# Kernel optimization log

Measured on AMD Instinct MI355X. Metric: run time of the kernel, lower is better.

## Reference

```python
import jax, jax.numpy as jnp
import numpy as np
import math

V, E, H, NL = 10000, 256, 512, 2
B, T = 64, 128


def _lstm_cell(x, h, c, Wih, Whh, b):
    # PyTorch gate order: i, f, g, o
    gates = x @ Wih.T + h @ Whh.T + b
    i, f, g, o = jnp.split(gates, 4, axis=-1)
    c = jax.nn.sigmoid(f) * c + jax.nn.sigmoid(i) * jnp.tanh(g)
    h = jax.nn.sigmoid(o) * jnp.tanh(c)
    return h, c


def _run_layer(xs, Wih, Whh, b):
    # xs: [T, B, D]; returns outputs [T, B, H] and final (h, c)
    Bn = xs.shape[1]
    h0 = jnp.zeros((Bn, H), xs.dtype)
    c0 = jnp.zeros((Bn, H), xs.dtype)

    def step(carry, x):
        h, c = carry
        h, c = _lstm_cell(x, h, c, Wih, Whh, b)
        return (h, c), h

    (hT, cT), ys = jax.lax.scan(step, (h0, c0), xs)
    return ys, hT, cT


def setup_inputs() -> dict:
    key = jax.random.key(0)
    ks = jax.random.split(key, 24)
    s = 0.05

    def n(k, shape):
        return jax.random.normal(k, shape, dtype=jnp.float32) * s

    inp = {
        "input_ids": jax.random.randint(ks[0], (B, T), 0, V),
        "my_attention_mask": jax.random.randint(ks[1], (B, T), 0, 2),
        "update_step": 1000,
        # encoder params
        "enc_embed": n(ks[2], (V, E)),
        "enc_Wih0": n(ks[3], (4 * H, E)),
        "enc_Whh0": n(ks[4], (4 * H, H)),
        "enc_b0": n(ks[5], (4 * H,)),
        "enc_Wih1": n(ks[6], (4 * H, H)),
        "enc_Whh1": n(ks[7], (4 * H, H)),
        "enc_b1": n(ks[8], (4 * H,)),
        # decoder params
        "dec_embed": n(ks[9], (V, E)),
        "dec_Wih0": n(ks[10], (4 * H, E)),
        "dec_Whh0": n(ks[11], (4 * H, H)),
        "dec_b0": n(ks[12], (4 * H,)),
        "dec_Wih1": n(ks[13], (4 * H, H)),
        "dec_Whh1": n(ks[14], (4 * H, H)),
        "dec_b1": n(ks[15], (4 * H,)),
        "dec_Wout": n(ks[16], (V, H)),
        "dec_bout": n(ks[17], (V,)),
    }
    return inp


def _forward(input_ids, my_attention_mask, update_step,
             enc_embed, enc_Wih0, enc_Whh0, enc_b0, enc_Wih1, enc_Whh1, enc_b1,
             dec_embed, dec_Wih0, dec_Whh0, dec_b0, dec_Wih1, dec_Whh1, dec_b1,
             dec_Wout, dec_bout):
    temp_ids = input_ids.T                      # [T, B]
    mask = my_attention_mask                    # [B, T]

    # ---- encoder: 2-layer LSTM over the full sequence ----
    emb = enc_embed[temp_ids]                   # [T, B, E]
    ys0, h0, c0 = _run_layer(emb, enc_Wih0, enc_Whh0, enc_b0)
    _, h1, c1 = _run_layer(ys0, enc_Wih1, enc_Whh1, enc_b1)

    def dec_step(carry, tok):
        dh0, dc0, dh1, dc1 = carry
        x = dec_embed[tok]                      # [B, E]
        dh0, dc0 = _lstm_cell(x, dh0, dc0, dec_Wih0, dec_Whh0, dec_b0)
        dh1, dc1 = _lstm_cell(dh0, dh1, dc1, dec_Wih1, dec_Whh1, dec_b1)
        out = dh1 @ dec_Wout.T + dec_bout       # [B, V]
        return (dh0, dc0, dh1, dc1), out

    _, dec_outs = jax.lax.scan(dec_step, (h0, c0, h1, c1), temp_ids[:-1])  # [T-1, B, V]

    # ---- mask-driven compaction: outputs[i, j] = dec_out at t where
    #      i = exclusive-cumsum of mask[j, :t]; unwritten slots stay random ----
    outputs = jax.random.uniform(jax.random.key(42), (T, B, V), dtype=jnp.float32)
    idx = jnp.cumsum(mask, axis=1) - mask       # exclusive cumsum, [B, T]
    write_i = jnp.where(mask[:, 1:] > 0, idx[:, 1:], T)   # OOB -> dropped
    vals = jnp.transpose(dec_outs, (1, 0, 2))   # [B, T-1, V]
    outputs = outputs.at[write_i, jnp.arange(B)[:, None]].set(vals, mode="drop")

    # ---- hard gumbel-softmax with straight-through ----
    temperature = max(0.5, math.exp(-0.003 * update_step))
    eps = 1e-20
    U = jax.random.uniform(jax.random.key(7), (T, B, V), dtype=jnp.float32)
    g = -jnp.log(-jnp.log(U + eps) + eps)
    y = jax.nn.softmax((outputs + g) / temperature, axis=-1)
    y_hard = jax.nn.one_hot(jnp.argmax(y, axis=-1), V, dtype=y.dtype)
    gs = jax.lax.stop_gradient(y_hard - y) + y  # [T, B, V]

    # ---- scatter back into padded layout: masked positions pull compacted
    #      gumbel onehots, unmasked positions get onehot(input id) ----
    gathered = gs[jnp.clip(idx, 0, T - 1), jnp.arange(B)[:, None]]  # [B, T, V]
    id_onehot = jax.nn.one_hot(input_ids, V, dtype=jnp.float32)     # [B, T, V]
    onehots = jnp.where((mask > 0)[:, :, None], gathered, id_onehot)
    return onehots.reshape(B * T, V)


def reference(input_ids, my_attention_mask, update_step,
              enc_embed, enc_Wih0, enc_Whh0, enc_b0, enc_Wih1, enc_Whh1, enc_b1,
              dec_embed, dec_Wih0, dec_Whh0, dec_b0, dec_Wih1, dec_Whh1, dec_b1,
              dec_Wout, dec_bout):
    return _forward(input_ids, my_attention_mask, update_step,
                    enc_embed, enc_Wih0, enc_Whh0, enc_b0, enc_Wih1, enc_Whh1, enc_b1,
                    dec_embed, dec_Wih0, dec_Whh0, dec_b0, dec_Wih1, dec_Whh1, dec_b1,
                    dec_Wout, dec_bout)
```

## Files before the change

kernel.cpp:

```cpp
#include <hip/hip_runtime.h>
#include <stdint.h>


#define RNG_VARIANT 2

__device__ __forceinline__ void threefry2x32(uint32_t k0, uint32_t k1,
                                             uint32_t x0, uint32_t x1,
                                             uint32_t& o0, uint32_t& o1)
{
  const uint32_t k2 = k0 ^ k1 ^ 0x1BD11BDAu;
  x0 += k0; x1 += k1;
#define TF_R(r) x0 += x1; x1 = (x1 << r) | (x1 >> (32 - r)); x1 ^= x0;
  TF_R(13) TF_R(15) TF_R(26) TF_R(6)
  x0 += k1; x1 += k2 + 1u;
  TF_R(17) TF_R(29) TF_R(16) TF_R(24)
  x0 += k2; x1 += k0 + 2u;
  TF_R(13) TF_R(15) TF_R(26) TF_R(6)
  x0 += k0; x1 += k1 + 3u;
  TF_R(17) TF_R(29) TF_R(16) TF_R(24)
  x0 += k1; x1 += k2 + 4u;
  TF_R(13) TF_R(15) TF_R(26) TF_R(6)
  x0 += k2; x1 += k0 + 5u;
#undef TF_R
  o0 = x0; o1 = x1;
}

__device__ __forceinline__ float jax_uniform(uint32_t seed, uint32_t i)
{
  uint32_t bits;
#if RNG_VARIANT == 0
  const uint32_t HALF = 40960000u;
  const bool lo = (i < HALF);
  const uint32_t x0 = lo ? i : (i - HALF);
  uint32_t o0, o1;
  threefry2x32(0u, seed, x0, x0 + HALF, o0, o1);
  bits = lo ? o0 : o1;
#else
  uint32_t o0, o1;
  threefry2x32(0u, seed, 0u, i, o0, o1);
#if RNG_VARIANT == 1
  bits = o1;
#elif RNG_VARIANT == 2
  bits = o0 ^ o1;
#else
  bits = o0;
#endif
#endif
  return __uint_as_float(0x3F800000u | (bits >> 9)) - 1.0f;
}

__global__ __launch_bounds__(256)
void gemm_kernel(const float* __restrict__ A, const int* __restrict__ ids,
                 const float* __restrict__ W, const float* __restrict__ bias,
                 float* __restrict__ C, int M, int N, int K, int amode, int cmode)
{
  __shared__ __align__(16) float As[16][64];
  __shared__ __align__(16) float Bs[16][64];
  const int tid = threadIdx.x;
  const int tx = tid & 15;
  const int ty = tid >> 4;
  const int m0 = blockIdx.x * 64;
  const int n0 = blockIdx.y * 64;
  const int lm = tid >> 2;
  const int kq = tid & 3;

  const float* arow = nullptr;
  if (amode == 0) {
    const int m = m0 + lm;
    const int token = ids[(m & 63) * 128 + (m >> 6)];
    arow = A + (size_t)token * K;
  }
  const int nW = n0 + lm;
  const bool wok = (nW < N);
  const float* wrow = W + (size_t)(wok ? nW : 0) * K;

  float acc[4][4] = {{0.f,0.f,0.f,0.f},{0.f,0.f,0.f,0.f},
                     {0.f,0.f,0.f,0.f},{0.f,0.f,0.f,0.f}};

  for (int k0 = 0; k0 < K; k0 += 16) {
    if (amode == 0) {
      const float4 av = *(const float4*)(arow + k0 + kq * 4);
      As[kq*4+0][lm] = av.x; As[kq*4+1][lm] = av.y;
      As[kq*4+2][lm] = av.z; As[kq*4+3][lm] = av.w;
    } else {
      ((float4*)&As[0][0])[tid] =
          ((const float4*)(A + (size_t)m0 * K + (size_t)k0 * 64))[tid];
    }
    float4 wv = make_float4(0.f, 0.f, 0.f, 0.f);
    if (wok) wv = *(const float4*)(wrow + k0 + kq * 4);
    Bs[kq*4+0][lm] = wv.x; Bs[kq*4+1][lm] = wv.y;
    Bs[kq*4+2][lm] = wv.z; Bs[kq*4+3][lm] = wv.w;
    __syncthreads();
#pragma unroll
    for (int kk = 0; kk < 16; ++kk) {
      const float4 a4 = *(const float4*)&As[kk][ty * 4];
      const float4 b4 = *(const float4*)&Bs[kk][tx * 4];
      acc[0][0] += a4.x*b4.x; acc[0][1] += a4.x*b4.y; acc[0][2] += a4.x*b4.z; acc[0][3] += a4.x*b4.w;
      acc[1][0] += a4.y*b4.x; acc[1][1] += a4.y*b4.y; acc[1][2] += a4.y*b4.z; acc[1][3] += a4.y*b4.w;
      acc[2][0] += a4.z*b4.x; acc[2][1] += a4.z*b4.y; acc[2][2] += a4.z*b4.z; acc[2][3] += a4.z*b4.w;
      acc[3][0] += a4.w*b4.x; acc[3][1] += a4.w*b4.y; acc[3][2] += a4.w*b4.z; acc[3][3] += a4.w*b4.w;
    }
    __syncthreads();
  }

  if (cmode == 0) {
#pragma unroll
    for (int i = 0; i < 4; ++i) {
      const int m = m0 + ty * 4 + i;
#pragma unroll
      for (int j = 0; j < 4; ++j) {
        const int n = n0 + tx * 4 + j;
        if (n < N) C[(size_t)m * N + n] = acc[i][j] + bias[n];
      }
    }
  } else {
    float* cb = C + (size_t)m0 * N;
#pragma unroll
    for (int j = 0; j < 4; ++j) {
      const int n = n0 + tx * 4 + j;
      if (n < N) {
        const float bv = bias[n];
#pragma unroll
        for (int i = 0; i < 4; ++i)
          cb[(size_t)n * 64 + ty * 4 + i] = acc[i][j] + bv;
      }
    }
  }
}

__global__ __launch_bounds__(128)
void lstm_step_kernel(const float* __restrict__ Xg,
                      const float* __restrict__ hprev,
                      const float* __restrict__ Whh,
                      float* __restrict__ cstate,
                      float* __restrict__ hout)
{
  __shared__ __align__(16) float ws[8][512];
  __shared__ __align__(16) float hs[4096];
  const int tid = threadIdx.x;
  const int b = tid & 63;
  const int ui = tid >> 6;
  const int U0 = blockIdx.x * 2;
  const int u = U0 + ui;

  {
    const int r = tid >> 4;
    const int lui = r >> 2, lg = r & 3;
    const float* wrow = Whh + (size_t)(lg * 512 + U0 + lui) * 512;
    const int kq = tid & 15;
#pragma unroll
    for (int i = 0; i < 8; ++i) {
      const int k = kq * 4 + i * 64;
      *(float4*)&ws[r][k] = *(const float4*)(wrow + k);
    }
  }

  const float x_i = Xg[(size_t)(0 * 512 + u) * 64 + b];
  const float x_f = Xg[(size_t)(1 * 512 + u) * 64 + b];
  const float x_g = Xg[(size_t)(2 * 512 + u) * 64 + b];
  const float x_o = Xg[(size_t)(3 * 512 + u) * 64 + b];
  const float c_old = cstate[(size_t)u * 64 + b];

  float4 pre[8];
#pragma unroll
  for (int i = 0; i < 8; ++i) pre[i] = ((const float4*)hprev)[tid + 128 * i];

  float a0 = 0.f, a1 = 0.f, a2 = 0.f, a3 = 0.f;
  for (int kc = 0; kc < 8; ++kc) {
    __syncthreads();
#pragma unroll
    for (int i = 0; i < 8; ++i) ((float4*)hs)[tid + 128 * i] = pre[i];
    __syncthreads();
    if (kc < 7) {
#pragma unroll
      for (int i = 0; i < 8; ++i)
        pre[i] = ((const float4*)hprev)[(kc + 1) * 1024 + tid + 128 * i];
    }
    const int kb = kc * 64;
#pragma unroll
    for (int kg = 0; kg < 16; ++kg) {
      const float h0 = hs[(kg * 4 + 0) * 64 + b];
      const float h1 = hs[(kg * 4 + 1) * 64 + b];
      const float h2 = hs[(kg * 4 + 2) * 64 + b];
      const float h3 = hs[(kg * 4 + 3) * 64 + b];
      const float4 w0 = *(const float4*)&ws[ui * 4 + 0][kb + kg * 4];
      const float4 w1 = *(const float4*)&ws[ui * 4 + 1][kb + kg * 4];
      const float4 w2 = *(const float4*)&ws[ui * 4 + 2][kb + kg * 4];
      const float4 w3 = *(const float4*)&ws[ui * 4 + 3][kb + kg * 4];
      a0 += h0 * w0.x + h1 * w0.y + h2 * w0.z + h3 * w0.w;
      a1 += h0 * w1.x + h1 * w1.y + h2 * w1.z + h3 * w1.w;
      a2 += h0 * w2.x + h1 * w2.y + h2 * w2.z + h3 * w2.w;
      a3 += h0 * w3.x + h1 * w3.y + h2 * w3.z + h3 * w3.w;
    }
  }

  const float zi = x_i + a0, zf = x_f + a1, zg = x_g + a2, zo = x_o + a3;
  const float I = 1.0f / (1.0f + expf(-zi));
  const float F = 1.0f / (1.0f + expf(-zf));
  const float G = tanhf(zg);
  const float O = 1.0f / (1.0f + expf(-zo));
  const float cn = F * c_old + I * G;
  cstate[(size_t)u * 64 + b] = cn;
  hout[(size_t)u * 64 + b] = O * tanhf(cn);
}

__global__ __launch_bounds__(256)
void token_kernel(const int* __restrict__ input_ids,
                  const int* __restrict__ mask,
                  const float* __restrict__ logits,
                  int* __restrict__ tokens)
{
  const int row = blockIdx.x;
  const int b = row >> 7;
  const int t = row & 127;
  const int tid = threadIdx.x;
  const int mk = mask[row];
  if (mk == 0) {
    if (tid == 0) tokens[row] = input_ids[row];
    return;
  }
  int r = 0;
  for (int s = 0; s < t; ++s) r += mask[(b << 7) + s];

  const uint32_t base7  = (uint32_t)(r * 64 + b) * 10000u;
  const uint32_t base42 = (uint32_t)b * 10000u;
  const size_t loff = (t >= 1) ? (size_t)((t - 1) * 64 + b) * 10000u : 0u;
  const float* lrow = logits + loff;

  float best = -3.0e38f;
  int bestv = 0;
  for (int v = tid; v < 10000; v += 256) {
    const float u7 = jax_uniform(7u, base7 + (uint32_t)v);
    const float g = -logf(-logf(u7 + 1e-20f) + 1e-20f);
    float z = (t >= 1) ? lrow[v] : jax_uniform(42u, base42 + (uint32_t)v);
    z += g;
    if (z > best) { best = z; bestv = v; }
  }
  __shared__ float sv[256];
  __shared__ int sidx[256];
  sv[tid] = best; sidx[tid] = bestv;
  __syncthreads();
  for (int s = 128; s > 0; s >>= 1) {
    if (tid < s) {
      const float ov = sv[tid + s]; const int oi = sidx[tid + s];
      if (ov > sv[tid] || (ov == sv[tid] && oi < sidx[tid])) {
        sv[tid] = ov; sidx[tid] = oi;
      }
    }
    __syncthreads();
  }
  if (tid == 0) tokens[row] = sidx[0];
}

__global__ __launch_bounds__(256)
void onehot_kernel(const int* __restrict__ tokens, float* __restrict__ out)
{
  const int row = blockIdx.x;
  const int tok = tokens[row];
  float4* orow = (float4*)(out + (size_t)row * 10000);
  for (int q = threadIdx.x; q < 2500; q += 256) {
    float4 v = make_float4(0.f, 0.f, 0.f, 0.f);
    const int v0 = q << 2;
    const unsigned d = (unsigned)(tok - v0);
    if (d < 4u) ((float*)&v)[d] = 1.0f;
    orow[q] = v;
  }
}

__global__ __launch_bounds__(256)
void zero_kernel(float* __restrict__ p, int n)
{
  const int i = blockIdx.x * 256 + threadIdx.x;
  if (i < n) p[i] = 0.f;
}

extern "C" void kernel_launch(void* const* d_in, const int* in_sizes, int n_in,
                              void* d_out, int out_size, void* d_ws, size_t ws_size,
                              hipStream_t stream)
{
  const int*   input_ids = (const int*)d_in[0];
  const int*   mask      = (const int*)d_in[1];
  const float* enc_embed = (const float*)d_in[3];
  const float* enc_Wih0  = (const float*)d_in[4];
  const float* enc_Whh0  = (const float*)d_in[5];
  const float* enc_b0    = (const float*)d_in[6];
  const float* enc_Wih1  = (const float*)d_in[7];
  const float* enc_Whh1  = (const float*)d_in[8];
  const float* enc_b1    = (const float*)d_in[9];
  const float* dec_embed = (const float*)d_in[10];
  const float* dec_Wih0  = (const float*)d_in[11];
  const float* dec_Whh0  = (const float*)d_in[12];
  const float* dec_b0    = (const float*)d_in[13];
  const float* dec_Wih1  = (const float*)d_in[14];
  const float* dec_Whh1  = (const float*)d_in[15];
  const float* dec_b1    = (const float*)d_in[16];
  const float* dec_Wout  = (const float*)d_in[17];
  const float* dec_bout  = (const float*)d_in[18];

  float* outf = (float*)d_out;
  float* Xg   = outf;
  float* seqA = (float*)d_ws;
  float* zbuf = seqA + (size_t)128 * 32768;
  float* cA   = zbuf + 32768;
  float* cB   = cA + 32768;
  float* hp0  = cB + 32768;
  float* hp1  = hp0 + 32768;
  int* tokens = (int*)(hp1 + 32768);

  zero_kernel<<<384, 256, 0, stream>>>(zbuf, 3 * 32768);

  gemm_kernel<<<dim3(128, 32), 256, 0, stream>>>(
      enc_embed, input_ids, enc_Wih0, enc_b0, Xg, 8192, 2048, 256, 0, 1);
  for (int t = 0; t < 128; ++t) {
    const float* hi = (t == 0) ? zbuf : (seqA + (size_t)(t - 1) * 32768);
    lstm_step_kernel<<<256, 128, 0, stream>>>(
        Xg + (size_t)t * 131072, hi, enc_Whh0, cA, seqA + (size_t)t * 32768);
  }

  gemm_kernel<<<dim3(128, 32), 256, 0, stream>>>(
      seqA, nullptr, enc_Wih1, enc_b1, Xg, 8192, 2048, 512, 1, 1);
  for (int t = 0; t < 128; ++t) {
    const float* hi = (t == 0) ? zbuf : ((t & 1) ? hp0 : hp1);
    float* ho = (t & 1) ? hp1 : hp0;
    lstm_step_kernel<<<256, 128, 0, stream>>>(
        Xg + (size_t)t * 131072, hi, enc_Whh1, cB, ho);
  }

  gemm_kernel<<<dim3(127, 32), 256, 0, stream>>>(
      dec_embed, input_ids, dec_Wih0, dec_b0, Xg, 8128, 2048, 256, 0, 1);
  for (int j = 0; j < 127; ++j) {
    const float* hi = (j == 0) ? (seqA + (size_t)127 * 32768)
                               : (seqA + (size_t)(j - 1) * 32768);
    lstm_step_kernel<<<256, 128, 0, stream>>>(
        Xg + (size_t)j * 131072, hi, dec_Whh0, cA, seqA + (size_t)j * 32768);
  }

  gemm_kernel<<<dim3(127, 32), 256, 0, stream>>>(
      seqA, nullptr, dec_Wih1, dec_b1, Xg, 8128, 2048, 512, 1, 1);
  for (int j = 0; j < 127; ++j) {
    const float* hi = (j == 0) ? hp1 : (seqA + (size_t)(j - 1) * 32768);
    lstm_step_kernel<<<256, 128, 0, stream>>>(
        Xg + (size_t)j * 131072, hi, dec_Whh1, cB, seqA + (size_t)j * 32768);
  }

  gemm_kernel<<<dim3(127, 157), 256, 0, stream>>>(
      seqA, nullptr, dec_Wout, dec_bout, outf, 8128, 10000, 512, 1, 0);

  token_kernel<<<8192, 256, 0, stream>>>(input_ids, mask, outf, tokens);
  onehot_kernel<<<8192, 256, 0, stream>>>(tokens, outf);
}
```

Baseline: 12.85 ms.

## Use split-bf16 MFMA GEMMs and fuse Gumbel argmax into output projection

Replaces the fp32 SIMT GEMMs with MFMA bf16 GEMMs that split each fp32 operand into hi/lo bf16 parts and use three products to keep near-fp32 accuracy. The hidden-state sequences are transposed and split, and the weights and embeddings are pre-split every call. The output projection GEMM now fuses the Gumbel noise and argmax, combining per-tile winners through packed 64-bit atomicMax keys. This removes the 8128x10000 logits write and re-read and the separate token kernel. In exchange it adds split and transpose passes on every call, and tie-breaking or precision may differ slightly.

```diff
diff --git a/kernel.cpp b/kernel.cpp
--- a/kernel.cpp
+++ b/kernel.cpp
@@ -2,7 +2,8 @@
 #include <stdint.h>
 
 
-#define RNG_VARIANT 2
+typedef short bf16x8 __attribute__((ext_vector_type(8)));
+typedef float f32x4 __attribute__((ext_vector_type(4)));
 
 __device__ __forceinline__ void threefry2x32(uint32_t k0, uint32_t k1,
                                              uint32_t x0, uint32_t x1,
@@ -27,102 +28,187 @@
 
 __device__ __forceinline__ float jax_uniform(uint32_t seed, uint32_t i)
 {
-  uint32_t bits;
-#if RNG_VARIANT == 0
-  const uint32_t HALF = 40960000u;
-  const bool lo = (i < HALF);
-  const uint32_t x0 = lo ? i : (i - HALF);
-  uint32_t o0, o1;
-  threefry2x32(0u, seed, x0, x0 + HALF, o0, o1);
-  bits = lo ? o0 : o1;
-#else
   uint32_t o0, o1;
   threefry2x32(0u, seed, 0u, i, o0, o1);
-#if RNG_VARIANT == 1
-  bits = o1;
-#elif RNG_VARIANT == 2
-  bits = o0 ^ o1;
-#else
-  bits = o0;
-#endif
-#endif
+  const uint32_t bits = o0 ^ o1;
   return __uint_as_float(0x3F800000u | (bits >> 9)) - 1.0f;
 }
 
-__global__ __launch_bounds__(256)
-void gemm_kernel(const float* __restrict__ A, const int* __restrict__ ids,
-                 const float* __restrict__ W, const float* __restrict__ bias,
-                 float* __restrict__ C, int M, int N, int K, int amode, int cmode)
-{
-  __shared__ __align__(16) float As[16][64];
-  __shared__ __align__(16) float Bs[16][64];
+__device__ __forceinline__ ushort f2bf(float x)
+{
+  const uint32_t u = __float_as_uint(x);
+  const uint32_t r = u + 0x7FFFu + ((u >> 16) & 1u);
+  return (ushort)(r >> 16);
+}
+__device__ __forceinline__ float bf2f(ushort b)
+{
+  return __uint_as_float(((uint32_t)b) << 16);
+}
+
+__device__ __forceinline__ unsigned long long packkey(float f, int n)
+{
+  uint32_t u = __float_as_uint(f);
+  u = (u & 0x80000000u) ? ~u : (u | 0x80000000u);
+  return ((unsigned long long)u << 32) | (uint32_t)(0x7FFFFFFF - n);
+}
+
+__global__ __launch_bounds__(256)
+void split_kernel(const float* __restrict__ src, ushort* __restrict__ hi,
+                  ushort* __restrict__ lo, int n)
+{
+  const int i = blockIdx.x * 256 + threadIdx.x;
+  if (i < n) {
+    const float v = src[i];
+    const ushort h = f2bf(v);
+    hi[i] = h;
+    lo[i] = f2bf(v - bf2f(h));
+  }
+}
+
+__global__ __launch_bounds__(256)
+void transpose_split_kernel(const float* __restrict__ seq,
+                            ushort* __restrict__ Thi, ushort* __restrict__ Tlo)
+{
+  __shared__ float tile[128][65];
+  const int t = blockIdx.x >> 2;
+  const int kc = blockIdx.x & 3;
   const int tid = threadIdx.x;
-  const int tx = tid & 15;
-  const int ty = tid >> 4;
-  const int m0 = blockIdx.x * 64;
-  const int n0 = blockIdx.y * 64;
-  const int lm = tid >> 2;
-  const int kq = tid & 3;
-
-  const float* arow = nullptr;
-  if (amode == 0) {
-    const int m = m0 + lm;
-    const int token = ids[(m & 63) * 128 + (m >> 6)];
-    arow = A + (size_t)token * K;
-  }
-  const int nW = n0 + lm;
-  const bool wok = (nW < N);
-  const float* wrow = W + (size_t)(wok ? nW : 0) * K;
-
-  float acc[4][4] = {{0.f,0.f,0.f,0.f},{0.f,0.f,0.f,0.f},
-                     {0.f,0.f,0.f,0.f},{0.f,0.f,0.f,0.f}};
-
-  for (int k0 = 0; k0 < K; k0 += 16) {
-    if (amode == 0) {
-      const float4 av = *(const float4*)(arow + k0 + kq * 4);
-      As[kq*4+0][lm] = av.x; As[kq*4+1][lm] = av.y;
-      As[kq*4+2][lm] = av.z; As[kq*4+3][lm] = av.w;
+  const float* sbase = seq + (size_t)t * 32768 + (size_t)kc * 128 * 64;
+#pragma unroll
+  for (int it = 0; it < 32; ++it) {
+    const int idx = it * 256 + tid;
+    tile[idx >> 6][idx & 63] = sbase[idx];
+  }
+  __syncthreads();
+#pragma unroll
+  for (int it = 0; it < 32; ++it) {
+    const int idx = it * 256 + tid;
+    const int b = idx >> 7, k = idx & 127;
+    const float v = tile[k][b];
+    const size_t o = ((size_t)t * 64 + b) * 512 + kc * 128 + k;
+    const ushort h = f2bf(v);
+    Thi[o] = h;
+    Tlo[o] = f2bf(v - bf2f(h));
+  }
+}
+
+template <int GATHER, int FUSED>
+__global__ __launch_bounds__(256)
+void gemm_split(const ushort* __restrict__ Ahi, const ushort* __restrict__ Alo,
+                const int* __restrict__ ids,
+                const ushort* __restrict__ Whi, const ushort* __restrict__ Wlo,
+                const float* __restrict__ bias, float* __restrict__ Xg,
+                const int* __restrict__ mask, const int* __restrict__ idxmap,
+                unsigned long long* __restrict__ keys,
+                int M, int N, int K)
+{
+  const int tid = threadIdx.x;
+  const int wid = tid >> 6, lane = tid & 63;
+  const int lm = lane & 15, quad = lane >> 4;
+  const int m0 = blockIdx.x * 128 + (wid >> 1) * 64;
+  const int n0 = blockIdx.y * 128 + (wid & 1) * 64;
+  const int koff = quad * 8;
+
+  size_t offA[4];
+#pragma unroll
+  for (int mi = 0; mi < 4; ++mi) {
+    int m = m0 + mi * 16 + lm;
+    int mc = m < M ? m : (M - 1);
+    if (GATHER) {
+      const int tok = ids[(mc & 63) * 128 + (mc >> 6)];
+      offA[mi] = (size_t)tok * K;
     } else {
-      ((float4*)&As[0][0])[tid] =
-          ((const float4*)(A + (size_t)m0 * K + (size_t)k0 * 64))[tid];
-    }
-    float4 wv = make_float4(0.f, 0.f, 0.f, 0.f);
-    if (wok) wv = *(const float4*)(wrow + k0 + kq * 4);
-    Bs[kq*4+0][lm] = wv.x; Bs[kq*4+1][lm] = wv.y;
-    Bs[kq*4+2][lm] = wv.z; Bs[kq*4+3][lm] = wv.w;
-    __syncthreads();
-#pragma unroll
-    for (int kk = 0; kk < 16; ++kk) {
-      const float4 a4 = *(const float4*)&As[kk][ty * 4];
-      const float4 b4 = *(const float4*)&Bs[kk][tx * 4];
-      acc[0][0] += a4.x*b4.x; acc[0][1] += a4.x*b4.y; acc[0][2] += a4.x*b4.z; acc[0][3] += a4.x*b4.w;
-      acc[1][0] += a4.y*b4.x; acc[1][1] += a4.y*b4.y; acc[1][2] += a4.y*b4.z; acc[1][3] += a4.y*b4.w;
-      acc[2][0] += a4.z*b4.x; acc[2][1] += a4.z*b4.y; acc[2][2] += a4.z*b4.z; acc[2][3] += a4.z*b4.w;
-      acc[3][0] += a4.w*b4.x; acc[3][1] += a4.w*b4.y; acc[3][2] += a4.w*b4.z; acc[3][3] += a4.w*b4.w;
-    }
-    __syncthreads();
-  }
-
-  if (cmode == 0) {
-#pragma unroll
-    for (int i = 0; i < 4; ++i) {
-      const int m = m0 + ty * 4 + i;
-#pragma unroll
-      for (int j = 0; j < 4; ++j) {
-        const int n = n0 + tx * 4 + j;
-        if (n < N) C[(size_t)m * N + n] = acc[i][j] + bias[n];
+      offA[mi] = (size_t)mc * K;
+    }
+  }
+  size_t offB[4];
+#pragma unroll
+  for (int ni = 0; ni < 4; ++ni) {
+    int n = n0 + ni * 16 + lm;
+    int nc = n < N ? n : (N - 1);
+    offB[ni] = (size_t)nc * K;
+  }
+
+  f32x4 acc[4][4];
+#pragma unroll
+  for (int mi = 0; mi < 4; ++mi)
+#pragma unroll
+    for (int ni = 0; ni < 4; ++ni) acc[mi][ni] = (f32x4){0.f, 0.f, 0.f, 0.f};
+
+  for (int k0 = 0; k0 < K; k0 += 32) {
+    bf16x8 ah[4], al[4];
+#pragma unroll
+    for (int mi = 0; mi < 4; ++mi) {
+      ah[mi] = *(const bf16x8*)(Ahi + offA[mi] + k0 + koff);
+      al[mi] = *(const bf16x8*)(Alo + offA[mi] + k0 + koff);
+    }
+#pragma unroll
+    for (int ni = 0; ni < 4; ++ni) {
+      const bf16x8 bh = *(const bf16x8*)(Whi + offB[ni] + k0 + koff);
+      const bf16x8 bl = *(const bf16x8*)(Wlo + offB[ni] + k0 + koff);
+#pragma unroll
+      for (int mi = 0; mi < 4; ++mi) {
+        acc[mi][ni] = __builtin_amdgcn_mfma_f32_16x16x32_bf16(ah[mi], bl, acc[mi][ni], 0, 0, 0);
+        acc[mi][ni] = __builtin_amdgcn_mfma_f32_16x16x32_bf16(al[mi], bh, acc[mi][ni], 0, 0, 0);
+        acc[mi][ni] = __builtin_amdgcn_mfma_f32_16x16x32_bf16(ah[mi], bh, acc[mi][ni], 0, 0, 0);
       }
     }
+  }
+
+  float bv[4];
+#pragma unroll
+  for (int ni = 0; ni < 4; ++ni) {
+    int n = n0 + ni * 16 + lm;
+    bv[ni] = bias[n < N ? n : (N - 1)];
+  }
+
+  if (FUSED == 0) {
+#pragma unroll
+    for (int mi = 0; mi < 4; ++mi) {
+#pragma unroll
+      for (int i = 0; i < 4; ++i) {
+        const int m = m0 + mi * 16 + quad * 4 + i;
+        if (m >= M) continue;
+        const int t = m >> 6, b = m & 63;
+        float* base = Xg + (size_t)t * 131072 + b;
+#pragma unroll
+        for (int ni = 0; ni < 4; ++ni) {
+          const int n = n0 + ni * 16 + lm;
+          base[(size_t)n * 64] = acc[mi][ni][i] + bv[ni];
+        }
+      }
+    }
   } else {
-    float* cb = C + (size_t)m0 * N;
-#pragma unroll
-    for (int j = 0; j < 4; ++j) {
-      const int n = n0 + tx * 4 + j;
-      if (n < N) {
-        const float bv = bias[n];
-#pragma unroll
-        for (int i = 0; i < 4; ++i)
-          cb[(size_t)n * 64 + ty * 4 + i] = acc[i][j] + bv;
+#pragma unroll
+    for (int mi = 0; mi < 4; ++mi) {
+#pragma unroll
+      for (int i = 0; i < 4; ++i) {
+        const int m = m0 + mi * 16 + quad * 4 + i;
+        if (m >= M) continue;
+        const int j = m >> 6, b = m & 63;
+        const int outrow = b * 128 + j + 1;
+        if (mask[outrow] == 0) continue;
+        const int r = idxmap[outrow];
+        const uint32_t base7 = (uint32_t)(r * 64 + b) * 10000u;
+        float best = -3.0e38f;
+        int bestn = 0;
+#pragma unroll
+        for (int ni = 0; ni < 4; ++ni) {
+          const int n = n0 + ni * 16 + lm;
+          if (n < N) {
+            const float u7 = jax_uniform(7u, base7 + (uint32_t)n);
+            const float g = -logf(-logf(u7 + 1e-20f) + 1e-20f);
+            const float z = acc[mi][ni][i] + bv[ni] + g;
+            if (z > best) { best = z; bestn = n; }
+          }
+        }
+        unsigned long long key = packkey(best, bestn);
+#pragma unroll
+        for (int s = 1; s < 16; s <<= 1) {
+          const unsigned long long o = __shfl_xor(key, s, 64);
+          if (o > key) key = o;
+        }
+        if (lm == 0) atomicMax(keys + outrow, key);
       }
     }
   }
@@ -204,52 +290,55 @@
   hout[(size_t)u * 64 + b] = O * tanhf(cn);
 }
 
-__global__ __launch_bounds__(256)
-void token_kernel(const int* __restrict__ input_ids,
-                  const int* __restrict__ mask,
-                  const float* __restrict__ logits,
-                  int* __restrict__ tokens)
-{
-  const int row = blockIdx.x;
-  const int b = row >> 7;
-  const int t = row & 127;
+__global__ void maskscan_kernel(const int* __restrict__ mask,
+                                int* __restrict__ idxmap)
+{
+  const int b = threadIdx.x;
+  int run = 0;
+  for (int t = 0; t < 128; ++t) {
+    idxmap[b * 128 + t] = run;
+    run += mask[b * 128 + t];
+  }
+}
+
+__global__ __launch_bounds__(256)
+void t0_kernel(const int* __restrict__ mask, unsigned long long* __restrict__ keys)
+{
+  const int b = blockIdx.x;
+  const int row = b * 128;
+  if (mask[row] == 0) return;
   const int tid = threadIdx.x;
-  const int mk = mask[row];
-  if (mk == 0) {
-    if (tid == 0) tokens[row] = input_ids[row];
-    return;
-  }
-  int r = 0;
-  for (int s = 0; s < t; ++s) r += mask[(b << 7) + s];
-
-  const uint32_t base7  = (uint32_t)(r * 64 + b) * 10000u;
-  const uint32_t base42 = (uint32_t)b * 10000u;
-  const size_t loff = (t >= 1) ? (size_t)((t - 1) * 64 + b) * 10000u : 0u;
-  const float* lrow = logits + loff;
-
+  const uint32_t base = (uint32_t)b * 10000u;
   float best = -3.0e38f;
-  int bestv = 0;
+  int bestn = 0;
   for (int v = tid; v < 10000; v += 256) {
-    const float u7 = jax_uniform(7u, base7 + (uint32_t)v);
+    const float u42 = jax_uniform(42u, base + (uint32_t)v);
+    const float u7 = jax_uniform(7u, base + (uint32_t)v);
     const float g = -logf(-logf(u7 + 1e-20f) + 1e-20f);
-    float z = (t >= 1) ? lrow[v] : jax_uniform(42u, base42 + (uint32_t)v);
-    z += g;
-    if (z > best) { best = z; bestv = v; }
-  }
-  __shared__ float sv[256];
-  __shared__ int sidx[256];
-  sv[tid] = best; sidx[tid] = bestv;
+    const float z = u42 + g;
+    if (z > best) { best = z; bestn = v; }
+  }
+  __shared__ unsigned long long sk[256];
+  sk[tid] = packkey(best, bestn);
   __syncthreads();
   for (int s = 128; s > 0; s >>= 1) {
-    if (tid < s) {
-      const float ov = sv[tid + s]; const int oi = sidx[tid + s];
-      if (ov > sv[tid] || (ov == sv[tid] && oi < sidx[tid])) {
-        sv[tid] = ov; sidx[tid] = oi;
-      }
-    }
+    if (tid < s) { if (sk[tid + s] > sk[tid]) sk[tid] = sk[tid + s]; }
     __syncthreads();
   }
-  if (tid == 0) tokens[row] = sidx[0];
+  if (tid == 0) keys[row] = sk[0];
+}
+
+__global__ __launch_bounds__(256)
+void finalize_kernel(const unsigned long long* __restrict__ keys,
+                     const int* __restrict__ mask,
+                     const int* __restrict__ input_ids,
+                     int* __restrict__ tokens)
+{
+  const int row = blockIdx.x * 256 + threadIdx.x;
+  if (row < 8192) {
+    tokens[row] = mask[row] ? (int)(0x7FFFFFFFu - (uint32_t)(keys[row] & 0xFFFFFFFFu))
+                            : input_ids[row];
+  }
 }
 
 __global__ __launch_bounds__(256)
@@ -297,8 +386,27 @@
   const float* dec_Wout  = (const float*)d_in[17];
   const float* dec_bout  = (const float*)d_in[18];
 
-  float* outf = (float*)d_out;
-  float* Xg   = outf;
+  char* O = (char*)d_out;
+  float*  Xg    = (float*)(O + 0);
+  ushort* sThi  = (ushort*)(O + 67108864);
+  ushort* sTlo  = (ushort*)(O + 75497472);
+  ushort* eEh   = (ushort*)(O + 83886080);
+  ushort* eEl   = (ushort*)(O + 89006080);
+  ushort* dEh   = (ushort*)(O + 94126080);
+  ushort* dEl   = (ushort*)(O + 99246080);
+  ushort* eW0h  = (ushort*)(O + 104366080);
+  ushort* eW0l  = (ushort*)(O + 105414656);
+  ushort* eW1h  = (ushort*)(O + 106463232);
+  ushort* eW1l  = (ushort*)(O + 108560384);
+  ushort* dW0h  = (ushort*)(O + 110657536);
+  ushort* dW0l  = (ushort*)(O + 111706112);
+  ushort* dW1h  = (ushort*)(O + 112754688);
+  ushort* dW1l  = (ushort*)(O + 114851840);
+  ushort* Woh   = (ushort*)(O + 116948992);
+  ushort* Wol   = (ushort*)(O + 127188992);
+  unsigned long long* keys = (unsigned long long*)(O + 137428992);
+  int*    idxmap = (int*)(O + 137494528);
+
   float* seqA = (float*)d_ws;
   float* zbuf = seqA + (size_t)128 * 32768;
   float* cA   = zbuf + 32768;
@@ -308,17 +416,30 @@
   int* tokens = (int*)(hp1 + 32768);
 
   zero_kernel<<<384, 256, 0, stream>>>(zbuf, 3 * 32768);
-
-  gemm_kernel<<<dim3(128, 32), 256, 0, stream>>>(
-      enc_embed, input_ids, enc_Wih0, enc_b0, Xg, 8192, 2048, 256, 0, 1);
+  zero_kernel<<<64, 256, 0, stream>>>((float*)keys, 16384);
+  maskscan_kernel<<<1, 64, 0, stream>>>(mask, idxmap);
+
+  split_kernel<<<10000, 256, 0, stream>>>(enc_embed, eEh, eEl, 2560000);
+  split_kernel<<<10000, 256, 0, stream>>>(dec_embed, dEh, dEl, 2560000);
+  split_kernel<<<2048, 256, 0, stream>>>(enc_Wih0, eW0h, eW0l, 524288);
+  split_kernel<<<4096, 256, 0, stream>>>(enc_Wih1, eW1h, eW1l, 1048576);
+  split_kernel<<<2048, 256, 0, stream>>>(dec_Wih0, dW0h, dW0l, 524288);
+  split_kernel<<<4096, 256, 0, stream>>>(dec_Wih1, dW1h, dW1l, 1048576);
+  split_kernel<<<20000, 256, 0, stream>>>(dec_Wout, Woh, Wol, 5120000);
+
+  gemm_split<1, 0><<<dim3(64, 16), 256, 0, stream>>>(
+      eEh, eEl, input_ids, eW0h, eW0l, enc_b0, Xg,
+      nullptr, nullptr, nullptr, 8192, 2048, 256);
   for (int t = 0; t < 128; ++t) {
     const float* hi = (t == 0) ? zbuf : (seqA + (size_t)(t - 1) * 32768);
     lstm_step_kernel<<<256, 128, 0, stream>>>(
         Xg + (size_t)t * 131072, hi, enc_Whh0, cA, seqA + (size_t)t * 32768);
   }
 
-  gemm_kernel<<<dim3(128, 32), 256, 0, stream>>>(
-      seqA, nullptr, enc_Wih1, enc_b1, Xg, 8192, 2048, 512, 1, 1);
+  transpose_split_kernel<<<512, 256, 0, stream>>>(seqA, sThi, sTlo);
+  gemm_split<0, 0><<<dim3(64, 16), 256, 0, stream>>>(
+      sThi, sTlo, nullptr, eW1h, eW1l, enc_b1, Xg,
+      nullptr, nullptr, nullptr, 8192, 2048, 512);
   for (int t = 0; t < 128; ++t) {
     const float* hi = (t == 0) ? zbuf : ((t & 1) ? hp0 : hp1);
     float* ho = (t & 1) ? hp1 : hp0;
@@ -326,8 +447,9 @@
         Xg + (size_t)t * 131072, hi, enc_Whh1, cB, ho);
   }
 
-  gemm_kernel<<<dim3(127, 32), 256, 0, stream>>>(
-      dec_embed, input_ids, dec_Wih0, dec_b0, Xg, 8128, 2048, 256, 0, 1);
+  gemm_split<1, 0><<<dim3(64, 16), 256, 0, stream>>>(
+      dEh, dEl, input_ids, dW0h, dW0l, dec_b0, Xg,
+      nullptr, nullptr, nullptr, 8128, 2048, 256);
   for (int j = 0; j < 127; ++j) {
     const float* hi = (j == 0) ? (seqA + (size_t)127 * 32768)
                                : (seqA + (size_t)(j - 1) * 32768);
@@ -335,17 +457,22 @@
         Xg + (size_t)j * 131072, hi, dec_Whh0, cA, seqA + (size_t)j * 32768);
   }
 
-  gemm_kernel<<<dim3(127, 32), 256, 0, stream>>>(
-      seqA, nullptr, dec_Wih1, dec_b1, Xg, 8128, 2048, 512, 1, 1);
+  transpose_split_kernel<<<508, 256, 0, stream>>>(seqA, sThi, sTlo);
+  gemm_split<0, 0><<<dim3(64, 16), 256, 0, stream>>>(
+      sThi, sTlo, nullptr, dW1h, dW1l, dec_b1, Xg,
+      nullptr, nullptr, nullptr, 8128, 2048, 512);
   for (int j = 0; j < 127; ++j) {
     const float* hi = (j == 0) ? hp1 : (seqA + (size_t)(j - 1) * 32768);
     lstm_step_kernel<<<256, 128, 0, stream>>>(
         Xg + (size_t)j * 131072, hi, dec_Whh1, cB, seqA + (size_t)j * 32768);
   }
 
-  gemm_kernel<<<dim3(127, 157), 256, 0, stream>>>(
-      seqA, nullptr, dec_Wout, dec_bout, outf, 8128, 10000, 512, 1, 0);
-
-  token_kernel<<<8192, 256, 0, stream>>>(input_ids, mask, outf, tokens);
-  onehot_kernel<<<8192, 256, 0, stream>>>(tokens, outf);
-}
+  transpose_split_kernel<<<508, 256, 0, stream>>>(seqA, sThi, sTlo);
+  gemm_split<0, 1><<<dim3(64, 79), 256, 0, stream>>>(
+      sThi, sTlo, nullptr, Woh, Wol, dec_bout, nullptr,
+      mask, idxmap, keys, 8128, 10000, 512);
+  t0_kernel<<<64, 256, 0, stream>>>(mask, keys);
+
+  finalize_kernel<<<32, 256, 0, stream>>>(keys, mask, input_ids, tokens);
+  onehot_kernel<<<8192, 256, 0, stream>>>(tokens, (float*)d_out);
+}
```

Result: faster. 12.06 ms (-6.1%).
